# Kernel optimization log

Measured on AMD Instinct MI355X. Metric: run time of the kernel, lower is better.

Reference implementation:

```python
import jax, jax.numpy as jnp
import numpy as np

N = 8192
IN_F = 64
OUT_F = 64
ALPHA = 0.2
NEG_INF = -9e15
DENSITY = 0.02


def _signed_sparse(key, shape, density):
    k1, k2 = jax.random.split(key)
    mask = jax.random.uniform(k1, shape) < density
    vals = jax.random.normal(k2, shape, dtype=jnp.float32)
    return jnp.where(mask, vals, 0.0)


def setup_inputs() -> dict:
    key = jax.random.key(0)
    k_h, k_na, k_ea, k_w, k_a = jax.random.split(key, 5)
    h = jax.random.normal(k_h, (N, IN_F), dtype=jnp.float32)
    node_adj = _signed_sparse(k_na, (N, N), DENSITY)
    edge_adj = _signed_sparse(k_ea, (N, N), DENSITY)
    # xavier_uniform with gain=1.414
    lim_w = 1.414 * np.sqrt(6.0 / (IN_F + OUT_F))
    W_att = jax.random.uniform(k_w, (IN_F, OUT_F), minval=-lim_w, maxval=lim_w, dtype=jnp.float32)
    lim_a = 1.414 * np.sqrt(6.0 / (OUT_F + 1))
    a = jax.random.uniform(k_a, (OUT_F, 1), minval=-lim_a, maxval=lim_a, dtype=jnp.float32)
    return {"h": h, "node_adj": node_adj, "edge_adj": edge_adj, "W_att": W_att, "a": a}


def reference(h, node_adj, edge_adj, W_att, a):
    # h: [N, F_in], node_adj/edge_adj: [N, N]
    h_att = h @ W_att                                   # [N, F_out]
    h_plus = (node_adj > 0).astype(h.dtype) @ h_att     # [N, F_out]
    h_minus = (node_adj < 0).astype(h.dtype) @ h_att    # [N, F_out]
    a_input = jnp.abs(h_plus - h_minus)                 # [N, F_out]
    e = jax.nn.leaky_relu(a_input @ a, ALPHA)           # [N, 1]
    e_row = e[:, 0][None, :]                            # broadcast: row i of scores = e^T
    scores = jnp.where(edge_adj != 0, e_row, jnp.float32(NEG_INF))  # [N, N]
    attention = jax.nn.softmax(scores, axis=1)          # [N, N]
    # dropout omitted (eval-mode reference)
    h_prime = (attention * edge_adj) @ h                # [N, F_in]
    return h_prime, attention
```

## Files before the change

kernel.cpp:

```cpp
#include <hip/hip_runtime.h>
#include <math.h>

#define NN 8192
#define FF 64
#define ALPHA 0.2f
#define ECAP 512
#define WCAP 256

__global__ __launch_bounds__(256) void k_hatt(const float* __restrict__ h,
                                              const float* __restrict__ W,
                                              float* __restrict__ h_att) {
    __shared__ float Ws[64 * 64];
    int t = threadIdx.x;
    for (int k = t; k < 64 * 64; k += 256) Ws[k] = W[k];
    __syncthreads();
    int idx = blockIdx.x * 256 + t;
    int r = idx >> 6, c = idx & 63;
    const float* hr = h + (size_t)r * FF;
    float acc = 0.f;
#pragma unroll
    for (int k = 0; k < 64; ++k) acc += hr[k] * Ws[k * 64 + c];
    h_att[idx] = acc;
}

__global__ __launch_bounds__(256) void k_e(const float* __restrict__ node_adj,
                                           const float* __restrict__ h_att,
                                           const float* __restrict__ a,
                                           float* __restrict__ e) {
    __shared__ int lists[4][ECAP];
    int t = threadIdx.x, w = t >> 6, lane = t & 63;
    int row = blockIdx.x * 4 + w;
    unsigned long long lmask = (1ull << lane) - 1ull;
    const float4* rp = (const float4*)(node_adj + (size_t)row * NN);
    int cnt = 0;
#pragma unroll 4
    for (int it = 0; it < 32; ++it) {
        int idx = it * 64 + lane;
        float4 v = rp[idx];
        int j0 = idx * 4;
        { bool nz = v.x != 0.f; unsigned long long m = __ballot(nz);
          if (nz) lists[w][cnt + __popcll(m & lmask)] = (v.x > 0.f) ? (j0 + 1) : -(j0 + 1);
          cnt += __popcll(m); }
        { bool nz = v.y != 0.f; unsigned long long m = __ballot(nz);
          if (nz) lists[w][cnt + __popcll(m & lmask)] = (v.y > 0.f) ? (j0 + 2) : -(j0 + 2);
          cnt += __popcll(m); }
        { bool nz = v.z != 0.f; unsigned long long m = __ballot(nz);
          if (nz) lists[w][cnt + __popcll(m & lmask)] = (v.z > 0.f) ? (j0 + 3) : -(j0 + 3);
          cnt += __popcll(m); }
        { bool nz = v.w != 0.f; unsigned long long m = __ballot(nz);
          if (nz) lists[w][cnt + __popcll(m & lmask)] = (v.w > 0.f) ? (j0 + 4) : -(j0 + 4);
          cnt += __popcll(m); }
    }
    __syncthreads();

    float acc = 0.f;
    for (int k = 0; k < cnt; ++k) {
        int code = lists[w][k];
        int j = (code < 0 ? -code : code) - 1;
        float hv = h_att[(size_t)j * FF + lane];
        acc += (code < 0) ? -hv : hv;
    }
    float v = fabsf(acc) * a[lane];
#pragma unroll
    for (int off = 32; off; off >>= 1) v += __shfl_down(v, off, 64);
    if (lane == 0) e[row] = (v > 0.f) ? v : ALPHA * v;
}

__global__ __launch_bounds__(256) void k_att(const float* __restrict__ edge_adj,
                                             const float* __restrict__ e,
                                             const float* __restrict__ h,
                                             float* __restrict__ att_out,
                                             float* __restrict__ hprime) {
    __shared__ int   jseg[4][WCAP];
    __shared__ float vseg[4][WCAP];
    __shared__ float red[256];
    __shared__ float r4m[4], r4z[4];
    __shared__ int   cnts[4];
    int t = threadIdx.x, w = t >> 6, lane = t & 63;
    int row = blockIdx.x;
    unsigned long long lmask = (1ull << lane) - 1ull;

    const float4* rp = (const float4*)(edge_adj + (size_t)row * NN);
    float4 rv[8];
    int cnt = 0;
#pragma unroll
    for (int it = 0; it < 8; ++it) {
        int idx = it * 256 + t;
        float4 v = rp[idx];
        rv[it] = v;
        int j0 = idx * 4;
        { bool nz = v.x != 0.f; unsigned long long m = __ballot(nz);
          if (nz) { int p = cnt + __popcll(m & lmask); jseg[w][p] = j0;     vseg[w][p] = v.x; }
          cnt += __popcll(m); }
        { bool nz = v.y != 0.f; unsigned long long m = __ballot(nz);
          if (nz) { int p = cnt + __popcll(m & lmask); jseg[w][p] = j0 + 1; vseg[w][p] = v.y; }
          cnt += __popcll(m); }
        { bool nz = v.z != 0.f; unsigned long long m = __ballot(nz);
          if (nz) { int p = cnt + __popcll(m & lmask); jseg[w][p] = j0 + 2; vseg[w][p] = v.z; }
          cnt += __popcll(m); }
        { bool nz = v.w != 0.f; unsigned long long m = __ballot(nz);
          if (nz) { int p = cnt + __popcll(m & lmask); jseg[w][p] = j0 + 3; vseg[w][p] = v.w; }
          cnt += __popcll(m); }
    }
    if (lane == 0) cnts[w] = cnt;
    __syncthreads();

    float mloc = -3.0e38f;
    for (int k = lane; k < cnt; k += 64) mloc = fmaxf(mloc, e[jseg[w][k]]);
#pragma unroll
    for (int off = 32; off; off >>= 1) mloc = fmaxf(mloc, __shfl_down(mloc, off, 64));
    if (lane == 0) r4m[w] = mloc;
    __syncthreads();
    float m = fmaxf(fmaxf(r4m[0], r4m[1]), fmaxf(r4m[2], r4m[3]));
    int tot = cnts[0] + cnts[1] + cnts[2] + cnts[3];

    float zloc = 0.f;
    for (int k = lane; k < cnt; k += 64) {
        float p = __expf(e[jseg[w][k]] - m);
        zloc += p;
        vseg[w][k] *= p;
    }
#pragma unroll
    for (int off = 32; off; off >>= 1) zloc += __shfl_down(zloc, off, 64);
    if (lane == 0) r4z[w] = zloc;
    __syncthreads();
    float Z = r4z[0] + r4z[1] + r4z[2] + r4z[3];
    float invZ = (tot > 0) ? 1.f / Z : 0.f;

    float acc = 0.f;
    for (int k = 0; k < cnt; ++k)
        acc += vseg[w][k] * h[(size_t)jseg[w][k] * FF + lane];
    red[t] = acc;
    __syncthreads();
    if (t < 64)
        hprime[(size_t)row * FF + t] = (red[t] + red[t + 64] + red[t + 128] + red[t + 192]) * invZ;

    const float4* ep = (const float4*)e;
    float4* ap = (float4*)(att_out + (size_t)row * NN);
    float unif = 1.0f / NN;
#pragma unroll
    for (int it = 0; it < 8; ++it) {
        int idx = it * 256 + t;
        float4 v = rv[it];
        float4 ev = ep[idx];
        float4 o;
        o.x = (v.x != 0.f) ? __expf(ev.x - m) * invZ : 0.f;
        o.y = (v.y != 0.f) ? __expf(ev.y - m) * invZ : 0.f;
        o.z = (v.z != 0.f) ? __expf(ev.z - m) * invZ : 0.f;
        o.w = (v.w != 0.f) ? __expf(ev.w - m) * invZ : 0.f;
        if (tot == 0) { o.x = unif; o.y = unif; o.z = unif; o.w = unif; }
        ap[idx] = o;
    }
}

extern "C" void kernel_launch(void* const* d_in, const int* in_sizes, int n_in,
                              void* d_out, int out_size, void* d_ws, size_t ws_size,
                              hipStream_t stream) {
    const float* h        = (const float*)d_in[0];
    const float* node_adj = (const float*)d_in[1];
    const float* edge_adj = (const float*)d_in[2];
    const float* W_att    = (const float*)d_in[3];
    const float* a        = (const float*)d_in[4];

    float* out    = (float*)d_out;
    float* hprime = out;
    float* att    = out + (size_t)NN * FF;

    float* h_att = (float*)d_ws;
    float* e_vec = h_att + (size_t)NN * FF;

    k_hatt<<<(NN * FF) / 256, 256, 0, stream>>>(h, W_att, h_att);
    k_e<<<NN / 4, 256, 0, stream>>>(node_adj, h_att, a, e_vec);
    k_att<<<NN, 256, 0, stream>>>(edge_adj, e_vec, h, att, hprime);
}
```

Before: 659.5 us.

## Precompute global-max exponentials to drop per-row softmax max pass; use nontemporal loads/stores

Adds a small kernel that takes the global max of e and precomputes exp(e - globalmax) once per column. The attention kernel then builds the numerator, the normalizer and the products in one streaming pass, with no per-row max reduction, extra barriers or per-element exp. Loads of the adjacency matrices and stores of the attention matrix become nontemporal. Using a global rather than per-row max risks underflow when a row's entries sit far below the global max, and it adds one kernel launch.

```diff
diff --git a/kernel.cpp b/kernel.cpp
--- a/kernel.cpp
+++ b/kernel.cpp
@@ -6,6 +6,8 @@
 #define ALPHA 0.2f
 #define ECAP 512
 #define WCAP 256
+
+typedef float vf4 __attribute__((ext_vector_type(4)));
 
 __global__ __launch_bounds__(256) void k_hatt(const float* __restrict__ h,
                                               const float* __restrict__ W,
@@ -31,12 +33,12 @@
     int t = threadIdx.x, w = t >> 6, lane = t & 63;
     int row = blockIdx.x * 4 + w;
     unsigned long long lmask = (1ull << lane) - 1ull;
-    const float4* rp = (const float4*)(node_adj + (size_t)row * NN);
+    const vf4* rp = (const vf4*)(node_adj + (size_t)row * NN);
     int cnt = 0;
 #pragma unroll 4
     for (int it = 0; it < 32; ++it) {
         int idx = it * 64 + lane;
-        float4 v = rp[idx];
+        vf4 v = __builtin_nontemporal_load(rp + idx);
         int j0 = idx * 4;
         { bool nz = v.x != 0.f; unsigned long long m = __ballot(nz);
           if (nz) lists[w][cnt + __popcll(m & lmask)] = (v.x > 0.f) ? (j0 + 1) : -(j0 + 1);
@@ -66,65 +68,68 @@
     if (lane == 0) e[row] = (v > 0.f) ? v : ALPHA * v;
 }
 
+__global__ __launch_bounds__(256) void k_prep(const float* __restrict__ e,
+                                              float* __restrict__ E) {
+    __shared__ float red[256];
+    int t = threadIdx.x;
+    float lm = -3.0e38f;
+    for (int k = t; k < NN; k += 256) lm = fmaxf(lm, e[k]);
+    red[t] = lm; __syncthreads();
+    for (int s = 128; s; s >>= 1) { if (t < s) red[t] = fmaxf(red[t], red[t + s]); __syncthreads(); }
+    float m = red[0];
+    int i = blockIdx.x * 256 + t;
+    E[i] = __expf(e[i] - m);
+}
+
 __global__ __launch_bounds__(256) void k_att(const float* __restrict__ edge_adj,
-                                             const float* __restrict__ e,
+                                             const float* __restrict__ E,
                                              const float* __restrict__ h,
                                              float* __restrict__ att_out,
                                              float* __restrict__ hprime) {
     __shared__ int   jseg[4][WCAP];
     __shared__ float vseg[4][WCAP];
     __shared__ float red[256];
-    __shared__ float r4m[4], r4z[4];
+    __shared__ float r4z[4];
     __shared__ int   cnts[4];
     int t = threadIdx.x, w = t >> 6, lane = t & 63;
     int row = blockIdx.x;
     unsigned long long lmask = (1ull << lane) - 1ull;
 
-    const float4* rp = (const float4*)(edge_adj + (size_t)row * NN);
-    float4 rv[8];
+    const vf4* rp = (const vf4*)(edge_adj + (size_t)row * NN);
+    const vf4* Ep = (const vf4*)E;
+    vf4 o[8];
+    float zloc = 0.f;
     int cnt = 0;
 #pragma unroll
     for (int it = 0; it < 8; ++it) {
         int idx = it * 256 + t;
-        float4 v = rp[idx];
-        rv[it] = v;
+        vf4 v  = __builtin_nontemporal_load(rp + idx);
+        vf4 Ev = Ep[idx];
         int j0 = idx * 4;
         { bool nz = v.x != 0.f; unsigned long long m = __ballot(nz);
-          if (nz) { int p = cnt + __popcll(m & lmask); jseg[w][p] = j0;     vseg[w][p] = v.x; }
-          cnt += __popcll(m); }
+          float ox = nz ? Ev.x : 0.f;
+          if (nz) { int p = cnt + __popcll(m & lmask); jseg[w][p] = j0;     vseg[w][p] = v.x * Ev.x; }
+          cnt += __popcll(m); zloc += ox; o[it].x = ox; }
         { bool nz = v.y != 0.f; unsigned long long m = __ballot(nz);
-          if (nz) { int p = cnt + __popcll(m & lmask); jseg[w][p] = j0 + 1; vseg[w][p] = v.y; }
-          cnt += __popcll(m); }
+          float oy = nz ? Ev.y : 0.f;
+          if (nz) { int p = cnt + __popcll(m & lmask); jseg[w][p] = j0 + 1; vseg[w][p] = v.y * Ev.y; }
+          cnt += __popcll(m); zloc += oy; o[it].y = oy; }
         { bool nz = v.z != 0.f; unsigned long long m = __ballot(nz);
-          if (nz) { int p = cnt + __popcll(m & lmask); jseg[w][p] = j0 + 2; vseg[w][p] = v.z; }
-          cnt += __popcll(m); }
+          float oz = nz ? Ev.z : 0.f;
+          if (nz) { int p = cnt + __popcll(m & lmask); jseg[w][p] = j0 + 2; vseg[w][p] = v.z * Ev.z; }
+          cnt += __popcll(m); zloc += oz; o[it].z = oz; }
         { bool nz = v.w != 0.f; unsigned long long m = __ballot(nz);
-          if (nz) { int p = cnt + __popcll(m & lmask); jseg[w][p] = j0 + 3; vseg[w][p] = v.w; }
-          cnt += __popcll(m); }
+          float ow = nz ? Ev.w : 0.f;
+          if (nz) { int p = cnt + __popcll(m & lmask); jseg[w][p] = j0 + 3; vseg[w][p] = v.w * Ev.w; }
+          cnt += __popcll(m); zloc += ow; o[it].w = ow; }
     }
     if (lane == 0) cnts[w] = cnt;
-    __syncthreads();
-
-    float mloc = -3.0e38f;
-    for (int k = lane; k < cnt; k += 64) mloc = fmaxf(mloc, e[jseg[w][k]]);
-#pragma unroll
-    for (int off = 32; off; off >>= 1) mloc = fmaxf(mloc, __shfl_down(mloc, off, 64));
-    if (lane == 0) r4m[w] = mloc;
-    __syncthreads();
-    float m = fmaxf(fmaxf(r4m[0], r4m[1]), fmaxf(r4m[2], r4m[3]));
-    int tot = cnts[0] + cnts[1] + cnts[2] + cnts[3];
-
-    float zloc = 0.f;
-    for (int k = lane; k < cnt; k += 64) {
-        float p = __expf(e[jseg[w][k]] - m);
-        zloc += p;
-        vseg[w][k] *= p;
-    }
 #pragma unroll
     for (int off = 32; off; off >>= 1) zloc += __shfl_down(zloc, off, 64);
     if (lane == 0) r4z[w] = zloc;
     __syncthreads();
     float Z = r4z[0] + r4z[1] + r4z[2] + r4z[3];
+    int tot = cnts[0] + cnts[1] + cnts[2] + cnts[3];
     float invZ = (tot > 0) ? 1.f / Z : 0.f;
 
     float acc = 0.f;
@@ -135,21 +140,15 @@
     if (t < 64)
         hprime[(size_t)row * FF + t] = (red[t] + red[t + 64] + red[t + 128] + red[t + 192]) * invZ;
 
-    const float4* ep = (const float4*)e;
-    float4* ap = (float4*)(att_out + (size_t)row * NN);
+    vf4* ap = (vf4*)(att_out + (size_t)row * NN);
     float unif = 1.0f / NN;
 #pragma unroll
     for (int it = 0; it < 8; ++it) {
         int idx = it * 256 + t;
-        float4 v = rv[it];
-        float4 ev = ep[idx];
-        float4 o;
-        o.x = (v.x != 0.f) ? __expf(ev.x - m) * invZ : 0.f;
-        o.y = (v.y != 0.f) ? __expf(ev.y - m) * invZ : 0.f;
-        o.z = (v.z != 0.f) ? __expf(ev.z - m) * invZ : 0.f;
-        o.w = (v.w != 0.f) ? __expf(ev.w - m) * invZ : 0.f;
-        if (tot == 0) { o.x = unif; o.y = unif; o.z = unif; o.w = unif; }
-        ap[idx] = o;
+        vf4 ov = o[it];
+        ov.x *= invZ; ov.y *= invZ; ov.z *= invZ; ov.w *= invZ;
+        if (tot == 0) { ov.x = unif; ov.y = unif; ov.z = unif; ov.w = unif; }
+        __builtin_nontemporal_store(ov, ap + idx);
     }
 }
 
@@ -168,8 +167,10 @@
 
     float* h_att = (float*)d_ws;
     float* e_vec = h_att + (size_t)NN * FF;
+    float* E_vec = e_vec + NN;
 
     k_hatt<<<(NN * FF) / 256, 256, 0, stream>>>(h, W_att, h_att);
     k_e<<<NN / 4, 256, 0, stream>>>(node_adj, h_att, a, e_vec);
-    k_att<<<NN, 256, 0, stream>>>(edge_adj, e_vec, h, att, hprime);
+    k_prep<<<NN / 256, 256, 0, stream>>>(e_vec, E_vec);
+    k_att<<<NN, 256, 0, stream>>>(edge_adj, E_vec, h, att, hprime);
 }
```

Result: faster. 628.1 us, median of 2 (-4.8%).
